# Kernel tuning notes

Measured on AMD Instinct MI355X. Metric: run time of the kernel, lower is better.

Reference implementation:

```python
import jax, jax.numpy as jnp
import numpy as np

NUM_HEADS = 8

def rotate_half(x):
    # interleaved rotate: pairs (x0,x1)->(-x1,x0)
    x1 = x[..., ::2]
    x2 = x[..., 1::2]
    return jnp.stack((-x2, x1), axis=-1).reshape(x.shape)

def rope_cos_sin(seq_len, head_dim, dtype, base=10000.0):
    idx = jnp.arange(0, head_dim, 2, dtype=dtype)
    inv_freq = 1.0 / base ** (idx / head_dim)
    t = jnp.arange(seq_len, dtype=dtype)
    freqs = t[:, None] * inv_freq[None, :]            # (L, hd/2)
    emb = jnp.concatenate([freqs, freqs], axis=-1)    # (L, hd) -- NOTE: cat, not interleave (faithful to source)
    return jnp.cos(emb)[None, None], jnp.sin(emb)[None, None]  # (1,1,L,hd)

def setup_inputs() -> dict:
    key = jax.random.key(0)
    ks = jax.random.split(key, 5)
    B, L, C = 2, 4096, 512
    s_in = 1.0 / np.sqrt(C)
    return {
        "x": jax.random.normal(ks[0], (B, L, C), dtype=jnp.float32),
        "qkv_w": jax.random.normal(ks[1], (3 * C, C), dtype=jnp.float32) * s_in,
        "qkv_b": jnp.zeros((3 * C,), dtype=jnp.float32),
        "proj_w": jax.random.normal(ks[2], (C, C), dtype=jnp.float32) * s_in,
        "proj_b": jnp.zeros((C,), dtype=jnp.float32),
    }

def reference(x, qkv_w, qkv_b, proj_w, proj_b):
    B, L, C = x.shape
    H = NUM_HEADS
    hd = C // H
    scale = hd ** -0.5
    qkv = x @ qkv_w.T + qkv_b                          # (B,L,3C)
    qkv = qkv.reshape(B, L, 3, H, hd).transpose(2, 0, 3, 1, 4)  # (3,B,H,L,hd)
    q, k, v = qkv[0], qkv[1], qkv[2]
    cos, sin = rope_cos_sin(L, hd, x.dtype)
    q = q * cos + rotate_half(q) * sin
    k = k * cos + rotate_half(k) * sin
    attn = jnp.einsum('bhqd,bhkd->bhqk', q, k) * scale  # (B,H,L,L)
    attn = jax.nn.softmax(attn, axis=-1)
    out = jnp.einsum('bhqk,bhkd->bhqd', attn, v)        # (B,H,L,hd)
    out = out.transpose(0, 2, 1, 3).reshape(B, L, C)
    return out @ proj_w.T + proj_b
```

## Files before the change

kernel.cpp:

```cpp
#include <hip/hip_runtime.h>
#include <hip/hip_bf16.h>


typedef __attribute__((ext_vector_type(8)))  short short8;
typedef __attribute__((ext_vector_type(4)))  short short4v;
typedef __attribute__((ext_vector_type(4)))  float floatx4;
typedef __attribute__((ext_vector_type(16))) float floatx16;

#define MFMA(a, b, c)   __builtin_amdgcn_mfma_f32_16x16x32_bf16((a), (b), (c), 0, 0, 0)
#define MFMA32(a, b, c) __builtin_amdgcn_mfma_f32_32x32x16_bf16((a), (b), (c), 0, 0, 0)

__device__ __forceinline__ float fast_exp2(float x) {
#if __has_builtin(__builtin_amdgcn_exp2f)
    return __builtin_amdgcn_exp2f(x);
#else
    float r; asm("v_exp_f32 %0, %1" : "=v"(r) : "v"(x)); return r;
#endif
}

__device__ __forceinline__ unsigned short f2bf(float f) {
    unsigned int u = __builtin_bit_cast(unsigned int, f);
    return (unsigned short)((u + 0x7fffu + ((u >> 16) & 1u)) >> 16);
}
__device__ __forceinline__ unsigned int pack2(float lo, float hi) {
    __hip_bfloat162 h = __float22bfloat162_rn(make_float2(lo, hi));
    unsigned int r;
    __builtin_memcpy(&r, &h, 4);
    return r;
}

__global__ __launch_bounds__(256) void conv_pack(
    const float* __restrict__ src, ushort* __restrict__ dst, int n8)
{
    int i = blockIdx.x * blockDim.x + threadIdx.x;
    if (i >= n8) return;
    const int row = i >> 6, col0 = (i & 63) * 8;
    const float4* s = (const float4*)(src + (size_t)row * 512 + col0);
    float4 a = s[0], b = s[1];
    uint4 r = { pack2(a.x, a.y), pack2(a.z, a.w), pack2(b.x, b.y), pack2(b.z, b.w) };
    const int l = (row & 15) + 16 * ((col0 >> 3) & 3);
    const size_t off = (size_t)(row >> 4) * 8192 + (size_t)(col0 >> 5) * 512 + l * 8;
    *(uint4*)(dst + off) = r;
}

__global__ __launch_bounds__(256) void build_rope(float2* __restrict__ lut) {
    int i = blockIdx.x * 256 + threadIdx.x;
    int pos = i >> 5, j = i & 31;
    float invf = exp2f(-0.41524101186f * (float)j);
    float s, c;
    sincosf((float)pos * invf, &s, &c);
    lut[i] = make_float2(c, s);
}

__global__ __launch_bounds__(256) void qkv_rope(
    const ushort* __restrict__ xb,
    const ushort* __restrict__ wb,
    const float* __restrict__ bias,
    const float2* __restrict__ lut,
    ushort* __restrict__ q, ushort* __restrict__ k, ushort* __restrict__ vt,
    int G, int h0)
{
    __shared__ __align__(16) ushort vtile[64][136];
    const int w_id = threadIdx.x >> 6;
    const int lane = threadIdx.x & 63;
    const int lr = lane & 15, quad = lane >> 4;
    const int m0 = blockIdx.x * 128 + w_id * 32;
    const int sec = blockIdx.y / G, hl = blockIdx.y % G;
    const int wc0 = sec * 512 + (h0 + hl) * 64;

    floatx4 acc[2][4] = {};
    const ushort* xa = xb + (size_t)(m0 >> 4) * 8192 + lane * 8;
    const ushort* wbase = wb + (size_t)(wc0 >> 4) * 8192 + lane * 8;
    for (int kk = 0; kk < 16; ++kk) {
        short8 a0 = *(const short8*)(xa + kk * 512);
        short8 a1 = *(const short8*)(xa + 8192 + kk * 512);
#pragma unroll
        for (int nt = 0; nt < 4; ++nt) {
            short8 b = *(const short8*)(wbase + (size_t)nt * 8192 + kk * 512);
            acc[0][nt] = MFMA(a0, b, acc[0][nt]);
            acc[1][nt] = MFMA(a1, b, acc[1][nt]);
        }
    }

    if (sec < 2) {
#pragma unroll
        for (int mt = 0; mt < 2; ++mt)
#pragma unroll
            for (int nt = 0; nt < 4; ++nt) {
                const int d = nt * 16 + lr;
                const float bv = bias[wc0 + d];
#pragma unroll
                for (int r = 0; r < 4; ++r) {
                    const int row = m0 + mt * 16 + quad * 4 + r;
                    const int b_ = row >> 12;
                    const int pos = row & 4095;
                    float val = acc[mt][nt][r] + bv;
                    const size_t bhl = (size_t)(b_ * G + hl);
                    float partner = __shfl_xor(val, 1);
                    float2 cs = lut[(pos << 5) | (d & 31)];
                    float rh = (d & 1) ? partner : -partner;
                    float rv = val * cs.x + rh * cs.y;
                    if (sec == 0) {
                        rv *= 0.18033688011112042f;
                        q[(bhl * 4096 + pos) * 64 + d] = f2bf(rv);
                    } else {
                        const int idx = (pos >> 5) * 2048 + (d >> 4) * 512
                                      + ((pos & 31) + 32 * ((d >> 3) & 1)) * 8
                                      + (d & 7);
                        k[bhl * 262144 + idx] = f2bf(rv);
                    }
                }
            }
    } else {
#pragma unroll
        for (int mt = 0; mt < 2; ++mt)
#pragma unroll
            for (int nt = 0; nt < 4; ++nt) {
                const int d = nt * 16 + lr;
                const float bv = bias[wc0 + d];
                short4v v4;
#pragma unroll
                for (int r = 0; r < 4; ++r)
                    v4[r] = (short)f2bf(acc[mt][nt][r] + bv);
                *(short4v*)&vtile[d][w_id * 32 + mt * 16 + quad * 4] = v4;
            }
        __syncthreads();
        const int m0b = blockIdx.x * 128;
        const int bb = m0b >> 12;
        const int c0g = (m0b & 4095) >> 5;
        const size_t bhl = (size_t)(bb * G + hl);
        const int gid = threadIdx.x >> 6;
        const int l = threadIdx.x & 63;
        const int h = l >> 5;
        ushort* vb = vt + bhl * 262144 + l * 8;
#pragma unroll
        for (int i = 0; i < 4; ++i) {
            const int combo = i * 4 + gid;
            const int c4 = combo >> 2, dt = (combo >> 1) & 1, s = combo & 1;
            const int d = dt * 32 + (l & 31);
            const int colbase = c4 * 32 + s * 16 + 4 * h;
            short4v a = *(const short4v*)&vtile[d][colbase];
            short4v b = *(const short4v*)&vtile[d][colbase + 8];
            short8 vv = __builtin_shufflevector(a, b, 0, 1, 2, 3, 4, 5, 6, 7);
            *(short8*)(vb + (size_t)(c0g + c4) * 2048 + dt * 1024 + s * 512) = vv;
        }
    }
}

__global__ __launch_bounds__(256, 3) void flash_attn(
    const ushort* __restrict__ q, const ushort* __restrict__ k,
    const ushort* __restrict__ vt, ushort* __restrict__ o,
    int G, int h0)
{
    __shared__ __align__(16) float mb[65][33];
    const int kh = threadIdx.x >> 6;
    const int lane = threadIdx.x & 63;
    const int ln31 = lane & 31, h = lane >> 5;
    const int nbh = 2 * G;
    const int bhl = blockIdx.x % nbh;
    const int qtile = blockIdx.x / nbh;
    const int b_ = bhl / G, hl = bhl % G;
    const int q0 = qtile * 32;

    const ushort* qp = q + (size_t)bhl * 262144;
    const int hcol = (h0 + hl) * 64;
    ushort* opp = o + (size_t)(((b_ << 12) + q0) >> 4) * 8192 + (hcol >> 5) * 512;
    const ushort* kpw = k + (size_t)bhl * 262144 + kh * 65536 + lane * 8;
    const ushort* vpw = vt + (size_t)bhl * 262144 + kh * 65536 + lane * 8;

    short8 qf[4];
    {
        const ushort* qb = qp + (size_t)(q0 + ln31) * 64 + h * 8;
        qf[0] = *(const short8*)(qb);
        qf[1] = *(const short8*)(qb + 16);
        qf[2] = *(const short8*)(qb + 32);
        qf[3] = *(const short8*)(qb + 48);
    }

    floatx16 oacc[2] = {};
    float lsum = 0.f;
    short8 ka0[4], ka1[4];
    short8 va[4];

    auto ldK = [&](int c, short8 (&ka)[4]) {
        const ushort* kb = kpw + c * 2048;
        ka[0] = *(const short8*)(kb);
        ka[1] = *(const short8*)(kb + 512);
        ka[2] = *(const short8*)(kb + 1024);
        ka[3] = *(const short8*)(kb + 1536);
    };
    auto ldV = [&](int c) {
        const ushort* vb = vpw + c * 2048;
        va[0] = *(const short8*)(vb);
        va[1] = *(const short8*)(vb + 512);
        va[2] = *(const short8*)(vb + 1024);
        va[3] = *(const short8*)(vb + 1536);
    };
    auto process = [&](short8 (&ka)[4]) {
        floatx16 s = {};
        s = MFMA32(ka[0], qf[0], s);
        s = MFMA32(ka[1], qf[1], s);
        s = MFMA32(ka[2], qf[2], s);
        s = MFMA32(ka[3], qf[3], s);
        float p[16];
#pragma unroll
        for (int r = 0; r < 16; ++r) p[r] = fast_exp2(s[r]);
        float t0 = (p[0] + p[1]) + (p[2] + p[3]);
        float t1 = (p[4] + p[5]) + (p[6] + p[7]);
        float t2 = (p[8] + p[9]) + (p[10] + p[11]);
        float t3 = (p[12] + p[13]) + (p[14] + p[15]);
        lsum += (t0 + t1) + (t2 + t3);
        uint4 u0 = { pack2(p[0], p[1]), pack2(p[2], p[3]),
                     pack2(p[4], p[5]), pack2(p[6], p[7]) };
        uint4 u1 = { pack2(p[8], p[9]), pack2(p[10], p[11]),
                     pack2(p[12], p[13]), pack2(p[14], p[15]) };
        short8 pb0 = __builtin_bit_cast(short8, u0);
        short8 pb1 = __builtin_bit_cast(short8, u1);
        oacc[0] = MFMA32(va[0], pb0, oacc[0]);
        oacc[0] = MFMA32(va[1], pb1, oacc[0]);
        oacc[1] = MFMA32(va[2], pb0, oacc[1]);
        oacc[1] = MFMA32(va[3], pb1, oacc[1]);
    };

    ldK(0, ka0);
    for (int it = 0; it < 30; it += 2) {
        ldV(it);
        ldK(it + 1, ka1);
        process(ka0);
        ldV(it + 1);
        ldK(it + 2, ka0);
        process(ka1);
    }
    ldV(30); ldK(31, ka1); process(ka0);
    ldV(31); process(ka1);

    lsum += __shfl_xor(lsum, 32);

    __syncthreads();
    if (kh == 3) {
#pragma unroll
        for (int dt = 0; dt < 2; ++dt)
#pragma unroll
            for (int r = 0; r < 16; ++r)
                mb[dt * 32 + (r & 3) + 8 * (r >> 2) + 4 * h][ln31] = oacc[dt][r];
        if (h == 0) mb[64][ln31] = lsum;
    }
    __syncthreads();
    if (kh == 2) {
#pragma unroll
        for (int dt = 0; dt < 2; ++dt)
#pragma unroll
            for (int r = 0; r < 16; ++r)
                mb[dt * 32 + (r & 3) + 8 * (r >> 2) + 4 * h][ln31] += oacc[dt][r];
        if (h == 0) mb[64][ln31] += lsum;
    }
    __syncthreads();
    if (kh == 1) {
#pragma unroll
        for (int dt = 0; dt < 2; ++dt)
#pragma unroll
            for (int r = 0; r < 16; ++r)
                mb[dt * 32 + (r & 3) + 8 * (r >> 2) + 4 * h][ln31] += oacc[dt][r];
        if (h == 0) mb[64][ln31] += lsum;
    }
    __syncthreads();
    if (kh == 0) {
        const float inv = 1.0f / (lsum + mb[64][ln31]);
#pragma unroll
        for (int dt = 0; dt < 2; ++dt)
#pragma unroll
            for (int g = 0; g < 4; ++g) {
                const int d0 = dt * 32 + 8 * g + 4 * h;
                float v0 = (oacc[dt][4 * g + 0] + mb[d0 + 0][ln31]) * inv;
                float v1 = (oacc[dt][4 * g + 1] + mb[d0 + 1][ln31]) * inv;
                float v2 = (oacc[dt][4 * g + 2] + mb[d0 + 2][ln31]) * inv;
                float v3 = (oacc[dt][4 * g + 3] + mb[d0 + 3][ln31]) * inv;
                uint2 u = { pack2(v0, v1), pack2(v2, v3) };
                *(uint2*)(opp + (size_t)(ln31 >> 4) * 8192 + dt * 512
                          + ((ln31 & 15) + 16 * g) * 8 + 4 * h) = u;
            }
    }
}

__global__ __launch_bounds__(256) void proj_gemm(
    const ushort* __restrict__ o,
    const ushort* __restrict__ wb,
    const float* __restrict__ bias,
    float* __restrict__ out)
{
    const int w_id = threadIdx.x >> 6;
    const int lane = threadIdx.x & 63;
    const int lr = lane & 15, quad = lane >> 4;
    const int m0 = blockIdx.x * 128 + w_id * 32;
    const int n0 = blockIdx.y * 64;

    floatx4 acc[2][4] = {};
    const ushort* oa = o + (size_t)(m0 >> 4) * 8192 + lane * 8;
    const ushort* wbase = wb + (size_t)(n0 >> 4) * 8192 + lane * 8;
    for (int kk = 0; kk < 16; ++kk) {
        short8 a0 = *(const short8*)(oa + kk * 512);
        short8 a1 = *(const short8*)(oa + 8192 + kk * 512);
#pragma unroll
        for (int nt = 0; nt < 4; ++nt) {
            short8 b = *(const short8*)(wbase + (size_t)nt * 8192 + kk * 512);
            acc[0][nt] = MFMA(a0, b, acc[0][nt]);
            acc[1][nt] = MFMA(a1, b, acc[1][nt]);
        }
    }
#pragma unroll
    for (int mt = 0; mt < 2; ++mt)
#pragma unroll
        for (int nt = 0; nt < 4; ++nt) {
            const int n = n0 + nt * 16 + lr;
            const float bv = bias[n];
#pragma unroll
            for (int r = 0; r < 4; ++r)
                out[(size_t)(m0 + mt * 16 + quad * 4 + r) * 512 + n] = acc[mt][nt][r] + bv;
        }
}

extern "C" void kernel_launch(void* const* d_in, const int* in_sizes, int n_in,
                              void* d_out, int out_size, void* d_ws, size_t ws_size,
                              hipStream_t stream)
{
    const float* x      = (const float*)d_in[0];
    const float* qkv_w  = (const float*)d_in[1];
    const float* qkv_b  = (const float*)d_in[2];
    const float* proj_w = (const float*)d_in[3];
    const float* proj_b = (const float*)d_in[4];
    float* out = (float*)d_out;

    const size_t MB = (size_t)1 << 20;
    ushort* base = (ushort*)d_ws;
    int G;
    ushort *xb, *o, *wb, *pwb, *q, *k, *vt;
    if (ws_size >= 34 * MB) {
        G = 8;
        xb = base; o = base;
        wb  = base + 4194304;
        pwb = wb + 786432;
        q   = pwb + 262144;
        k   = q + (size_t)G * 524288;
        vt  = k + (size_t)G * 524288;
    } else {
        G = (ws_size >= 30 * MB) ? 4 : (ws_size >= 24 * MB) ? 2 : 1;
        xb  = base;
        o   = base + 4194304;
        wb  = o + 4194304;
        pwb = wb + 786432;
        q   = pwb + 262144;
        k   = q + (size_t)G * 524288;
        vt  = k + (size_t)G * 524288;
    }

    float2* lut = (float2*)d_out;
    build_rope<<<512, 256, 0, stream>>>(lut);

    conv_pack<<<2048, 256, 0, stream>>>(x, xb, 524288);
    conv_pack<<<384, 256, 0, stream>>>(qkv_w, wb, 98304);
    conv_pack<<<128, 256, 0, stream>>>(proj_w, pwb, 32768);

    for (int h0 = 0; h0 < 8; h0 += G) {
        qkv_rope<<<dim3(64, 3 * G), 256, 0, stream>>>(xb, wb, qkv_b, lut, q, k, vt, G, h0);
        flash_attn<<<128 * 2 * G, 256, 0, stream>>>(q, k, vt, o, G, h0);
    }
    proj_gemm<<<dim3(64, 8), 256, 0, stream>>>(o, pwb, proj_b, out);
}
```

Baseline: 222.4 us.

## Share K/V tiles across four query-tile waves via double-buffered LDS

The flash attention kernel used to split the key range across four waves, each owning one 32-row query tile, and then merged their partial outputs through shared memory. Now each block handles 128 query rows, one 32-row tile per wave, and each wave walks all keys. K and V chunks are staged cooperatively into a double-buffered LDS tile so all four waves reuse them. This removes the cross-wave reduction and cuts global K/V traffic by four, at the cost of a barrier every chunk, a quarter as many blocks, and lower occupancy bounds.

```diff
diff --git a/kernel.cpp b/kernel.cpp
--- a/kernel.cpp
+++ b/kernel.cpp
@@ -147,26 +147,29 @@
     }
 }
 
-__global__ __launch_bounds__(256, 3) void flash_attn(
+__global__ __launch_bounds__(256, 2) void flash_attn(
     const ushort* __restrict__ q, const ushort* __restrict__ k,
     const ushort* __restrict__ vt, ushort* __restrict__ o,
     int G, int h0)
 {
-    __shared__ __align__(16) float mb[65][33];
-    const int kh = threadIdx.x >> 6;
+    __shared__ __align__(16) ushort kv[2][4096];
+    const int w_id = threadIdx.x >> 6;
     const int lane = threadIdx.x & 63;
     const int ln31 = lane & 31, h = lane >> 5;
     const int nbh = 2 * G;
     const int bhl = blockIdx.x % nbh;
-    const int qtile = blockIdx.x / nbh;
+    const int qt = blockIdx.x / nbh;
     const int b_ = bhl / G, hl = bhl % G;
-    const int q0 = qtile * 32;
+    const int q0 = qt * 128 + w_id * 32;
 
     const ushort* qp = q + (size_t)bhl * 262144;
+    const ushort* kp = k + (size_t)bhl * 262144;
+    const ushort* vp = vt + (size_t)bhl * 262144;
     const int hcol = (h0 + hl) * 64;
     ushort* opp = o + (size_t)(((b_ << 12) + q0) >> 4) * 8192 + (hcol >> 5) * 512;
-    const ushort* kpw = k + (size_t)bhl * 262144 + kh * 65536 + lane * 8;
-    const ushort* vpw = vt + (size_t)bhl * 262144 + kh * 65536 + lane * 8;
+
+    const ushort* stsrc = ((w_id < 2) ? kp : vp) + (w_id & 1) * 1024 + lane * 8;
+    const int stdst = w_id * 1024 + lane * 8;
 
     short8 qf[4];
     {
@@ -179,29 +182,23 @@
 
     floatx16 oacc[2] = {};
     float lsum = 0.f;
-    short8 ka0[4], ka1[4];
-    short8 va[4];
-
-    auto ldK = [&](int c, short8 (&ka)[4]) {
-        const ushort* kb = kpw + c * 2048;
-        ka[0] = *(const short8*)(kb);
-        ka[1] = *(const short8*)(kb + 512);
-        ka[2] = *(const short8*)(kb + 1024);
-        ka[3] = *(const short8*)(kb + 1536);
-    };
-    auto ldV = [&](int c) {
-        const ushort* vb = vpw + c * 2048;
-        va[0] = *(const short8*)(vb);
-        va[1] = *(const short8*)(vb + 512);
-        va[2] = *(const short8*)(vb + 1024);
-        va[3] = *(const short8*)(vb + 1536);
-    };
-    auto process = [&](short8 (&ka)[4]) {
+
+    auto process = [&](int cur) {
+        const ushort* kb = &kv[cur][lane * 8];
+        short8 ka0 = *(const short8*)(kb);
+        short8 ka1 = *(const short8*)(kb + 512);
+        short8 ka2 = *(const short8*)(kb + 1024);
+        short8 ka3 = *(const short8*)(kb + 1536);
+        const ushort* vb = kb + 2048;
+        short8 va0 = *(const short8*)(vb);
+        short8 va1 = *(const short8*)(vb + 512);
+        short8 va2 = *(const short8*)(vb + 1024);
+        short8 va3 = *(const short8*)(vb + 1536);
         floatx16 s = {};
-        s = MFMA32(ka[0], qf[0], s);
-        s = MFMA32(ka[1], qf[1], s);
-        s = MFMA32(ka[2], qf[2], s);
-        s = MFMA32(ka[3], qf[3], s);
+        s = MFMA32(ka0, qf[0], s);
+        s = MFMA32(ka1, qf[1], s);
+        s = MFMA32(ka2, qf[2], s);
+        s = MFMA32(ka3, qf[3], s);
         float p[16];
 #pragma unroll
         for (int r = 0; r < 16; ++r) p[r] = fast_exp2(s[r]);
@@ -216,70 +213,48 @@
                      pack2(p[12], p[13]), pack2(p[14], p[15]) };
         short8 pb0 = __builtin_bit_cast(short8, u0);
         short8 pb1 = __builtin_bit_cast(short8, u1);
-        oacc[0] = MFMA32(va[0], pb0, oacc[0]);
-        oacc[0] = MFMA32(va[1], pb1, oacc[0]);
-        oacc[1] = MFMA32(va[2], pb0, oacc[1]);
-        oacc[1] = MFMA32(va[3], pb1, oacc[1]);
+        oacc[0] = MFMA32(va0, pb0, oacc[0]);
+        oacc[0] = MFMA32(va1, pb1, oacc[0]);
+        oacc[1] = MFMA32(va2, pb0, oacc[1]);
+        oacc[1] = MFMA32(va3, pb1, oacc[1]);
     };
 
-    ldK(0, ka0);
-    for (int it = 0; it < 30; it += 2) {
-        ldV(it);
-        ldK(it + 1, ka1);
-        process(ka0);
-        ldV(it + 1);
-        ldK(it + 2, ka0);
-        process(ka1);
-    }
-    ldV(30); ldK(31, ka1); process(ka0);
-    ldV(31); process(ka1);
+    {
+        short8 t0 = *(const short8*)(stsrc);
+        short8 t1 = *(const short8*)(stsrc + 512);
+        *(short8*)(&kv[0][stdst]) = t0;
+        *(short8*)(&kv[0][stdst + 512]) = t1;
+    }
+    __syncthreads();
+
+    int cur = 0;
+    for (int c = 0; c < 127; ++c) {
+        const ushort* src = stsrc + (c + 1) * 2048;
+        short8 t0 = *(const short8*)(src);
+        short8 t1 = *(const short8*)(src + 512);
+        process(cur);
+        *(short8*)(&kv[cur ^ 1][stdst]) = t0;
+        *(short8*)(&kv[cur ^ 1][stdst + 512]) = t1;
+        __syncthreads();
+        cur ^= 1;
+    }
+    process(cur);
 
     lsum += __shfl_xor(lsum, 32);
 
-    __syncthreads();
-    if (kh == 3) {
-#pragma unroll
-        for (int dt = 0; dt < 2; ++dt)
-#pragma unroll
-            for (int r = 0; r < 16; ++r)
-                mb[dt * 32 + (r & 3) + 8 * (r >> 2) + 4 * h][ln31] = oacc[dt][r];
-        if (h == 0) mb[64][ln31] = lsum;
-    }
-    __syncthreads();
-    if (kh == 2) {
-#pragma unroll
-        for (int dt = 0; dt < 2; ++dt)
-#pragma unroll
-            for (int r = 0; r < 16; ++r)
-                mb[dt * 32 + (r & 3) + 8 * (r >> 2) + 4 * h][ln31] += oacc[dt][r];
-        if (h == 0) mb[64][ln31] += lsum;
-    }
-    __syncthreads();
-    if (kh == 1) {
-#pragma unroll
-        for (int dt = 0; dt < 2; ++dt)
-#pragma unroll
-            for (int r = 0; r < 16; ++r)
-                mb[dt * 32 + (r & 3) + 8 * (r >> 2) + 4 * h][ln31] += oacc[dt][r];
-        if (h == 0) mb[64][ln31] += lsum;
-    }
-    __syncthreads();
-    if (kh == 0) {
-        const float inv = 1.0f / (lsum + mb[64][ln31]);
-#pragma unroll
-        for (int dt = 0; dt < 2; ++dt)
-#pragma unroll
-            for (int g = 0; g < 4; ++g) {
-                const int d0 = dt * 32 + 8 * g + 4 * h;
-                float v0 = (oacc[dt][4 * g + 0] + mb[d0 + 0][ln31]) * inv;
-                float v1 = (oacc[dt][4 * g + 1] + mb[d0 + 1][ln31]) * inv;
-                float v2 = (oacc[dt][4 * g + 2] + mb[d0 + 2][ln31]) * inv;
-                float v3 = (oacc[dt][4 * g + 3] + mb[d0 + 3][ln31]) * inv;
-                uint2 u = { pack2(v0, v1), pack2(v2, v3) };
-                *(uint2*)(opp + (size_t)(ln31 >> 4) * 8192 + dt * 512
-                          + ((ln31 & 15) + 16 * g) * 8 + 4 * h) = u;
-            }
-    }
+    const float inv = 1.0f / lsum;
+#pragma unroll
+    for (int dt = 0; dt < 2; ++dt)
+#pragma unroll
+        for (int g = 0; g < 4; ++g) {
+            float v0 = oacc[dt][4 * g + 0] * inv;
+            float v1 = oacc[dt][4 * g + 1] * inv;
+            float v2 = oacc[dt][4 * g + 2] * inv;
+            float v3 = oacc[dt][4 * g + 3] * inv;
+            uint2 u = { pack2(v0, v1), pack2(v2, v3) };
+            *(uint2*)(opp + (size_t)(ln31 >> 4) * 8192 + dt * 512
+                      + ((ln31 & 15) + 16 * g) * 8 + 4 * h) = u;
+        }
 }
 
 __global__ __launch_bounds__(256) void proj_gemm(
@@ -362,7 +337,7 @@
 
     for (int h0 = 0; h0 < 8; h0 += G) {
         qkv_rope<<<dim3(64, 3 * G), 256, 0, stream>>>(xb, wb, qkv_b, lut, q, k, vt, G, h0);
-        flash_attn<<<128 * 2 * G, 256, 0, stream>>>(q, k, vt, o, G, h0);
+        flash_attn<<<32 * 2 * G, 256, 0, stream>>>(q, k, vt, o, G, h0);
     }
     proj_gemm<<<dim3(64, 8), 256, 0, stream>>>(o, pwb, proj_b, out);
 }
```

Result: faster. 210.8 us (-5.2%).
